# Performance work log

Measured on AMD Instinct MI355X. Metric: run time of the kernel, lower is better.

Reference implementation:

```python
import jax, jax.numpy as jnp
import numpy as np

N_HEADS = 12


def setup_inputs() -> dict:
    key = jax.random.key(0)
    ks = jax.random.split(key, 4)
    B, T, C = 1, 4096, 768
    x = jax.random.normal(ks[0], (B, T, C), dtype=jnp.float32)
    w_qkv = jax.random.normal(ks[1], (C, 3 * C), dtype=jnp.float32) * (C ** -0.5)
    b_qkv = jnp.zeros((3 * C,), dtype=jnp.float32)
    w_proj = jax.random.normal(ks[2], (C, C), dtype=jnp.float32) * (C ** -0.5)
    b_proj = jnp.zeros((C,), dtype=jnp.float32)
    return {"x": x, "w_qkv": w_qkv, "b_qkv": b_qkv, "w_proj": w_proj, "b_proj": b_proj}


def reference(x, w_qkv, b_qkv, w_proj, b_proj):
    B, T, C = x.shape
    H = N_HEADS
    hd = C // H
    qkv = x @ w_qkv + b_qkv                      # [B,T,3C]
    q, k, v = jnp.split(qkv, 3, axis=-1)
    # [B,H,T,hd]
    q = q.reshape(B, T, H, hd).transpose(0, 2, 1, 3)
    k = k.reshape(B, T, H, hd).transpose(0, 2, 1, 3)
    v = v.reshape(B, T, H, hd).transpose(0, 2, 1, 3)
    scale = 1.0 / jnp.sqrt(jnp.float32(hd))
    attn = jnp.einsum('bhqd,bhkd->bhqk', q, k) * scale  # [B,H,T,T]
    causal = jnp.tril(jnp.ones((T, T), dtype=bool))
    attn = jnp.where(causal, attn, jnp.float32(-jnp.inf))
    attn = jax.nn.softmax(attn, axis=-1)
    out = jnp.einsum('bhqk,bhkd->bhqd', attn, v)        # [B,H,T,hd]
    out = out.transpose(0, 2, 1, 3).reshape(B, T, C)
    return out @ w_proj + b_proj
```

## Files before the change

### kernel.cpp

```cpp
#include <hip/hip_runtime.h>
#include <hip/hip_bf16.h>


#define T_SEQ 4096
#define C_DIM 768
#define C3    2304
#define NH    12
#define HD    64

typedef __attribute__((ext_vector_type(8))) short bf16x8;
typedef __attribute__((ext_vector_type(4))) short bf16x4;
typedef __attribute__((ext_vector_type(4))) float f32x4;

__device__ inline unsigned short f2bf(float f) {
  union { float f; unsigned u; } v; v.f = f;
  unsigned r = v.u + 0x7fff + ((v.u >> 16) & 1);
  return (unsigned short)(r >> 16);
}
__device__ inline unsigned short f2bf_trunc(float f) {
  union { float f; unsigned u; } v; v.f = f;
  return (unsigned short)(v.u >> 16);
}

__device__ inline void gl2lds16(const void* g, void* l) {
  __builtin_amdgcn_global_load_lds(
      (const __attribute__((address_space(1))) unsigned int*)g,
      (__attribute__((address_space(3))) unsigned int*)l, 16, 0, 0);
}

#if __has_builtin(__builtin_amdgcn_exp2f)
#define EXP2F(x) __builtin_amdgcn_exp2f(x)
#else
#define EXP2F(x) exp2f(x)
#endif

#define NB_CONV  (T_SEQ * C_DIM / 2048)
#define NB_TQKV  ((C3 / 32) * (C_DIM / 32))
#define NB_TPROJ ((C_DIM / 32) * (C_DIM / 32))

__global__ __launch_bounds__(256) void prep_fused(
    const float* __restrict__ x, const float* __restrict__ w_qkv,
    const float* __restrict__ w_proj, unsigned short* __restrict__ xb,
    unsigned short* __restrict__ wqkvT, unsigned short* __restrict__ wprojT) {
  __shared__ float t[32][33];
  const int b = blockIdx.x;
  const int tid = threadIdx.x;

  if (b < NB_CONV) {
    int i = (b * 256 + tid) * 8;
    float4 v0 = *(const float4*)(x + i);
    float4 v1 = *(const float4*)(x + i + 4);
    unsigned short o[8] = {f2bf(v0.x), f2bf(v0.y), f2bf(v0.z), f2bf(v0.w),
                           f2bf(v1.x), f2bf(v1.y), f2bf(v1.z), f2bf(v1.w)};
    *(uint4*)(xb + i) = *(uint4*)o;
    return;
  }
  const float* in;
  unsigned short* outT;
  int R, Cc, bi;
  if (b < NB_CONV + NB_TQKV) {
    in = w_qkv; outT = wqkvT; R = C_DIM; Cc = C3; bi = b - NB_CONV;
  } else {
    in = w_proj; outT = wprojT; R = C_DIM; Cc = C_DIM; bi = b - NB_CONV - NB_TQKV;
  }
  const int tx = tid & 31, ty = tid >> 5;
  const int c0 = (bi % (Cc / 32)) * 32, r0 = (bi / (Cc / 32)) * 32;
#pragma unroll
  for (int i = 0; i < 4; ++i) {
    int r = ty + i * 8;
    t[r][tx] = in[(size_t)(r0 + r) * Cc + c0 + tx];
  }
  __syncthreads();
#pragma unroll
  for (int i = 0; i < 4; ++i) {
    int c = ty + i * 8;
    outT[(size_t)(c0 + c) * R + r0 + tx] = f2bf(t[tx][c]);
  }
}

__global__ __launch_bounds__(256) void gemm_qkv(
    const unsigned short* __restrict__ A, const unsigned short* __restrict__ Bt,
    const float* __restrict__ bias, unsigned short* __restrict__ Cq,
    unsigned short* __restrict__ vTp, int M, int N, int K) {
  __shared__ unsigned short As[128 * 64];
  __shared__ unsigned short Bs[128 * 64];
  const int tid = threadIdx.x;
  const int wave = tid >> 6, lane = tid & 63;
  const int lo = lane & 15, g8 = lane >> 4;
  const int lo7 = lo & 7;
  const int wm = wave >> 1, wn = wave & 1;
  const int bm = blockIdx.y * 128, bn = blockIdx.x * 128;
  const int drow8 = lane >> 3;
  const int dslot = (lane & 7) * 8;
  const int dsrc = ((lane & 7) ^ drow8) * 8;

  f32x4 acc[4][4];
#pragma unroll
  for (int mt = 0; mt < 4; ++mt)
#pragma unroll
    for (int nt = 0; nt < 4; ++nt) acc[mt][nt] = (f32x4){0.f, 0.f, 0.f, 0.f};

  const unsigned short* Abase = A + (size_t)bm * K;
  const unsigned short* Bbase = Bt + (size_t)bn * K;

  for (int k0 = 0; k0 < K; k0 += 64) {
    __syncthreads();
#pragma unroll
    for (int p = 0; p < 4; ++p) {
      const int r = p * 32 + wave * 8 + drow8;
      gl2lds16(Abase + (size_t)r * K + k0 + dsrc, As + r * 64 + dslot);
      gl2lds16(Bbase + (size_t)r * K + k0 + dsrc, Bs + r * 64 + dslot);
    }
    __syncthreads();

#pragma unroll
    for (int kk = 0; kk < 2; ++kk) {
      bf16x8 a[4], b[4];
#pragma unroll
      for (int mt = 0; mt < 4; ++mt)
        a[mt] = *(const bf16x8*)(
            As + (wm * 64 + mt * 16 + lo) * 64 + (((kk * 4 + g8) ^ lo7) * 8));
#pragma unroll
      for (int nt = 0; nt < 4; ++nt)
        b[nt] = *(const bf16x8*)(
            Bs + (wn * 64 + nt * 16 + lo) * 64 + (((kk * 4 + g8) ^ lo7) * 8));
#pragma unroll
      for (int mt = 0; mt < 4; ++mt)
#pragma unroll
        for (int nt = 0; nt < 4; ++nt)
          acc[mt][nt] = __builtin_amdgcn_mfma_f32_16x16x32_bf16(a[mt], b[nt], acc[mt][nt], 0, 0, 0);
    }
  }

  if (bn < 2 * C_DIM) {
#pragma unroll
    for (int nt = 0; nt < 4; ++nt) {
      const int n = bn + wn * 64 + nt * 16 + lo;
      const float bv = bias[n];
#pragma unroll
      for (int mt = 0; mt < 4; ++mt)
#pragma unroll
        for (int r = 0; r < 4; ++r) {
          const int m = bm + wm * 64 + mt * 16 + g8 * 4 + r;
          Cq[(size_t)m * C3 + n] = f2bf(acc[mt][nt][r] + bv);
        }
    }
  } else {
#pragma unroll
    for (int nt = 0; nt < 4; ++nt) {
      const int n = bn + wn * 64 + nt * 16 + lo;
      const float bv = bias[n];
      unsigned short* row = vTp + (size_t)(n - 2 * C_DIM) * T_SEQ;
#pragma unroll
      for (int mt = 0; mt < 4; ++mt) {
        const int mbase = (bm + wm * 64 + mt * 16 + g8 * 4) & ~31;
        bf16x4 o4;
#pragma unroll
        for (int r = 0; r < 4; ++r) o4[r] = (short)f2bf(acc[mt][nt][r] + bv);
        *(bf16x4*)(row + mbase + 8 * g8 + 4 * (mt & 1)) = o4;
      }
    }
  }
}

__global__ __launch_bounds__(256) void gemm_bt_mfma(
    const unsigned short* __restrict__ A, const unsigned short* __restrict__ Bt,
    const float* __restrict__ bias, float* __restrict__ C,
    int M, int N, int K) {
  __shared__ unsigned short As[128 * 64];
  __shared__ unsigned short Bs[128 * 64];
  const int tid = threadIdx.x;
  const int wave = tid >> 6, lane = tid & 63;
  const int lo = lane & 15, g8 = lane >> 4;
  const int lo7 = lo & 7;
  const int wm = wave >> 1, wn = wave & 1;
  const int bm = blockIdx.y * 128, bn = blockIdx.x * 128;
  const int drow8 = lane >> 3;
  const int dslot = (lane & 7) * 8;
  const int dsrc = ((lane & 7) ^ drow8) * 8;

  f32x4 acc[4][4];
#pragma unroll
  for (int mt = 0; mt < 4; ++mt)
#pragma unroll
    for (int nt = 0; nt < 4; ++nt) acc[mt][nt] = (f32x4){0.f, 0.f, 0.f, 0.f};

  const unsigned short* Abase = A + (size_t)bm * K;
  const unsigned short* Bbase = Bt + (size_t)bn * K;

  for (int k0 = 0; k0 < K; k0 += 64) {
    __syncthreads();
#pragma unroll
    for (int p = 0; p < 4; ++p) {
      const int r = p * 32 + wave * 8 + drow8;
      gl2lds16(Abase + (size_t)r * K + k0 + dsrc, As + r * 64 + dslot);
      gl2lds16(Bbase + (size_t)r * K + k0 + dsrc, Bs + r * 64 + dslot);
    }
    __syncthreads();

#pragma unroll
    for (int kk = 0; kk < 2; ++kk) {
      bf16x8 a[4], b[4];
#pragma unroll
      for (int mt = 0; mt < 4; ++mt)
        a[mt] = *(const bf16x8*)(
            As + (wm * 64 + mt * 16 + lo) * 64 + (((kk * 4 + g8) ^ lo7) * 8));
#pragma unroll
      for (int nt = 0; nt < 4; ++nt)
        b[nt] = *(const bf16x8*)(
            Bs + (wn * 64 + nt * 16 + lo) * 64 + (((kk * 4 + g8) ^ lo7) * 8));
#pragma unroll
      for (int mt = 0; mt < 4; ++mt)
#pragma unroll
        for (int nt = 0; nt < 4; ++nt)
          acc[mt][nt] = __builtin_amdgcn_mfma_f32_16x16x32_bf16(a[mt], b[nt], acc[mt][nt], 0, 0, 0);
    }
  }

#pragma unroll
  for (int nt = 0; nt < 4; ++nt) {
    const int n = bn + wn * 64 + nt * 16 + lo;
    const float bv = bias[n];
#pragma unroll
    for (int mt = 0; mt < 4; ++mt)
#pragma unroll
      for (int r = 0; r < 4; ++r) {
        const int m = bm + wm * 64 + mt * 16 + g8 * 4 + r;
        C[(size_t)m * N + n] = acc[mt][nt][r] + bv;
      }
  }
}

#define PO_SLOT ((size_t)NH * 64 * 4096)
#define PL_SLOT ((size_t)NH * 64 * 64)

__global__ __launch_bounds__(256) void flash_attn_split14(
    const unsigned short* __restrict__ qkv,
    const unsigned short* __restrict__ vTp,
    float* __restrict__ Po, float* __restrict__ Pl) {
  __shared__ unsigned short Ks[3][64 * 64];
  __shared__ unsigned short Vs[3][64 * 64];

  const int bid = blockIdx.x;
  const int xcd = bid & 7;
  const int j2 = bid >> 3;
  const int Hh = xcd * 3 + (j2 >> 5);
  const int h = Hh >> 1;
  const int s = Hh & 1;
  const int i = j2 & 31;
  const int j = 63 - i;
  const int nJ = s ? (31 - i) : 33;
  const int kJ0 = s ? 33 : 0;
  const int nI = s ? (i + 1) : 0;
  const int T = nJ + nI;

  const int tid = threadIdx.x;
  const int w = tid >> 6;
  const int lane = tid & 63;
  const int lo = lane & 15;
  const int g = lane >> 4;
  const int lo7 = lo & 7;
  const float qscale = 0.125f * 1.44269504f;

  const unsigned short* Kg = qkv + C_DIM + h * HD;
  const unsigned short* Vg = vTp + (size_t)(h * HD) * T_SEQ;

  const int drow = tid >> 3;
  const int dslot = (tid & 7) * 8;
  const int dsrc = ((tid & 7) ^ (drow & 7)) * 8;

  bf16x8 qbJ[2], qbI[2];
#pragma unroll
  for (int dh = 0; dh < 2; ++dh)
    qbJ[dh] = *(const bf16x8*)(
        qkv + (size_t)(j * 64 + w * 16 + lo) * C3 + h * HD + dh * 32 + g * 8);
#pragma unroll
  for (int dh = 0; dh < 2; ++dh)
    qbI[dh] = *(const bf16x8*)(
        qkv + (size_t)(i * 64 + w * 16 + lo) * C3 + h * HD + dh * 32 + g * 8);

  auto KT = [&](int t) { return t < nJ ? kJ0 + t : t - nJ; };

  {
    const int ka = KT(0), kb = KT(1);
#pragma unroll
    for (int p2 = 0; p2 < 2; ++p2) {
      const int r = p2 * 32 + drow;
      gl2lds16(Kg + (size_t)(ka * 64 + r) * C3 + dsrc, Ks[0] + r * 64 + dslot);
      gl2lds16(Vg + (size_t)r * T_SEQ + ka * 64 + dsrc, Vs[0] + r * 64 + dslot);
    }
#pragma unroll
    for (int p2 = 0; p2 < 2; ++p2) {
      const int r = p2 * 32 + drow;
      gl2lds16(Kg + (size_t)(kb * 64 + r) * C3 + dsrc, Ks[1] + r * 64 + dslot);
      gl2lds16(Vg + (size_t)r * T_SEQ + kb * 64 + dsrc, Vs[1] + r * 64 + dslot);
    }
    asm volatile("s_waitcnt vmcnt(4)" ::: "memory");
    __builtin_amdgcn_s_barrier();
  }

  float l_i = 0.f;
  f32x4 o_acc[4];
#pragma unroll
  for (int dt = 0; dt < 4; ++dt) o_acc[dt] = (f32x4){0.f, 0.f, 0.f, 0.f};

  int ic = 0;
  int iw = 2;
  int t = 0;

  auto body = [&](const bf16x8 (&qb)[2], int qtcur) __attribute__((always_inline)) {
    if (t + 2 < T) {
      const int k2 = KT(t + 2);
      unsigned short* Kd = Ks[iw];
      unsigned short* Vd = Vs[iw];
#pragma unroll
      for (int p2 = 0; p2 < 2; ++p2) {
        const int r = p2 * 32 + drow;
        gl2lds16(Kg + (size_t)(k2 * 64 + r) * C3 + dsrc, Kd + r * 64 + dslot);
        gl2lds16(Vg + (size_t)r * T_SEQ + k2 * 64 + dsrc, Vd + r * 64 + dslot);
      }
    }
    const unsigned short* Kc = Ks[ic];
    const unsigned short* Vc = Vs[ic];
    const int ktc = KT(t);

    f32x4 st[4];
#pragma unroll
    for (int mt = 0; mt < 4; ++mt) st[mt] = (f32x4){0.f, 0.f, 0.f, 0.f};
#pragma unroll
    for (int mt = 0; mt < 4; ++mt)
#pragma unroll
      for (int dh = 0; dh < 2; ++dh) {
        bf16x8 a = *(const bf16x8*)(
            Kc + (mt * 16 + lo) * 64 + (((dh * 4 + g) ^ lo7) * 8));
        st[mt] = __builtin_amdgcn_mfma_f32_16x16x32_bf16(a, qb[dh], st[mt], 0, 0, 0);
      }

    if (ktc == qtcur) {
      const int qloc = w * 16 + lo;
#pragma unroll
      for (int mt = 0; mt < 4; ++mt)
#pragma unroll
        for (int r = 0; r < 4; ++r)
          if (mt * 16 + g * 4 + r > qloc) st[mt][r] = -1e30f;
    }

    float lsum = 0.f;
    bf16x8 pt[2];
#pragma unroll
    for (int kh = 0; kh < 2; ++kh) {
#pragma unroll
      for (int jj = 0; jj < 4; ++jj) {
        float e0 = EXP2F(st[kh * 2][jj] * qscale);
        float e1 = EXP2F(st[kh * 2 + 1][jj] * qscale);
        lsum += e0 + e1;
        pt[kh][jj] = (short)f2bf_trunc(e0);
        pt[kh][4 + jj] = (short)f2bf_trunc(e1);
      }
    }
    l_i += lsum;

#pragma unroll
    for (int dt = 0; dt < 4; ++dt)
#pragma unroll
      for (int kh = 0; kh < 2; ++kh) {
        bf16x8 av = *(const bf16x8*)(
            Vc + (dt * 16 + lo) * 64 + (((kh * 4 + g) ^ lo7) * 8));
        o_acc[dt] = __builtin_amdgcn_mfma_f32_16x16x32_bf16(av, pt[kh], o_acc[dt], 0, 0, 0);
      }

    if (t + 2 < T)
      asm volatile("s_waitcnt vmcnt(4)" ::: "memory");
    else
      asm volatile("s_waitcnt vmcnt(0)" ::: "memory");
    __builtin_amdgcn_s_barrier();

    ic = (ic == 2) ? 0 : ic + 1;
    iw = (iw == 2) ? 0 : iw + 1;
    ++t;
  };

  auto flush = [&](int slot, int qt) __attribute__((always_inline)) {
    float lred = l_i + __shfl_xor(l_i, 16);
    lred += __shfl_xor(lred, 32);
    float* PoS = Po + ((size_t)slot * NH + h) * (64 * 4096) + (size_t)qt * 4096;
#pragma unroll
    for (int dt = 0; dt < 4; ++dt)
      *(f32x4*)(PoS + (w * 16 + lo) * 64 + dt * 16 + g * 4) = o_acc[dt];
    if (g == 0)
      Pl[(((size_t)slot * NH + h) * 64 + qt) * 64 + w * 16 + lo] = lred;
    l_i = 0.f;
#pragma unroll
    for (int dt = 0; dt < 4; ++dt) o_acc[dt] = (f32x4){0.f, 0.f, 0.f, 0.f};
  };

  for (int u = 0; u < nJ; ++u) body(qbJ, j);
  if (nJ > 0) flush(s, j);
  for (int u = 0; u < nI; ++u) body(qbI, i);
  if (nI > 0) flush(0, i);
}

__global__ __launch_bounds__(256) void combine_partials(
    const float* __restrict__ Po, const float* __restrict__ Pl,
    unsigned short* __restrict__ out) {
  const int bid = blockIdx.x;
  const int h = bid / 64, qt = bid % 64;
  const int tid = threadIdx.x;
  const int q = tid >> 2;
  const int c = (tid & 3) * 16;
  const bool two = (qt >= 33);
  const size_t sl = (size_t)h * 64 + qt;
  const float* P0 = Po + sl * 4096 + q * 64 + c;
  const float* P1 = P0 + PO_SLOT;
  float l = Pl[sl * 64 + q];
  if (two) l += Pl[PL_SLOT + sl * 64 + q];
  const float inv = 1.0f / l;
  unsigned short ob[16];
#pragma unroll
  for (int e = 0; e < 4; ++e) {
    f32x4 v = *(const f32x4*)(P0 + e * 4);
    if (two) {
      f32x4 v1 = *(const f32x4*)(P1 + e * 4);
      v += v1;
    }
#pragma unroll
    for (int r = 0; r < 4; ++r) ob[e * 4 + r] = f2bf(v[r] * inv);
  }
  unsigned short* o = out + (size_t)(qt * 64 + q) * C_DIM + h * 64 + c;
  *(uint4*)o = *(uint4*)ob;
  *(uint4*)(o + 8) = *(uint4*)(ob + 8);
}

extern "C" void kernel_launch(void* const* d_in, const int* in_sizes, int n_in,
                              void* d_out, int out_size, void* d_ws, size_t ws_size,
                              hipStream_t stream) {
  const float* x      = (const float*)d_in[0];
  const float* w_qkv  = (const float*)d_in[1];
  const float* b_qkv  = (const float*)d_in[2];
  const float* w_proj = (const float*)d_in[3];
  const float* b_proj = (const float*)d_in[4];
  float* out = (float*)d_out;

  unsigned short* xb     = (unsigned short*)d_ws;
  unsigned short* wqkvT  = xb + (size_t)T_SEQ * C_DIM;
  unsigned short* wprojT = wqkvT + (size_t)C3 * C_DIM;
  unsigned short* qkv    = wprojT + (size_t)C_DIM * C_DIM;
  unsigned short* vTp    = qkv + (size_t)T_SEQ * C3;
  unsigned short* attnb  = vTp + (size_t)C_DIM * T_SEQ;
  float* Po = (float*)(attnb + (size_t)T_SEQ * C_DIM);
  float* Pl = Po + 2 * PO_SLOT;

  prep_fused<<<NB_CONV + NB_TQKV + NB_TPROJ, 256, 0, stream>>>(
      x, w_qkv, w_proj, xb, wqkvT, wprojT);

  gemm_qkv<<<dim3(C3 / 128, T_SEQ / 128), 256, 0, stream>>>(
      xb, wqkvT, b_qkv, qkv, vTp, T_SEQ, C3, C_DIM);

  flash_attn_split14<<<T_SEQ / 64 * NH, 256, 0, stream>>>(qkv, vTp, Po, Pl);

  combine_partials<<<NH * 64, 256, 0, stream>>>(Po, Pl, attnb);

  gemm_bt_mfma<<<dim3(C_DIM / 128, T_SEQ / 128), 256, 0, stream>>>(
      attnb, wprojT, b_proj, out, T_SEQ, C_DIM, C_DIM);
}
```

Baseline: 180.6 us.

## Split attention work into three KV ranges per query pair with MFMA row sums

Attention work is re-split so each paired (i, 63-i) query-tile chain of 65 KV tiles is divided into three chunks of about 22 tiles. This gives 1152 blocks instead of 768, for better load balance and occupancy, and the combine step now merges up to three partials. The softmax scale and log2e are folded into Q in the QKV GEMM epilogue, and row sums are computed with an MFMA against a ones vector instead of scalar adds and shuffles. The LDS pipeline also drops from three to two buffers with full vmcnt(0) waits and adds s_setprio around the MFMA sections. The two-buffer pipeline exposes more load latency, and the extra partials increase combine traffic.

After: 186.4 us. 1.03x slower.

```diff
diff --git a/kernel.cpp b/kernel.cpp
--- a/kernel.cpp
+++ b/kernel.cpp
@@ -133,6 +133,7 @@
   }
 
   if (bn < 2 * C_DIM) {
+    const float sc = (bn < C_DIM) ? 0.18033688011112042f : 1.0f;
 #pragma unroll
     for (int nt = 0; nt < 4; ++nt) {
       const int n = bn + wn * 64 + nt * 16 + lo;
@@ -142,7 +143,7 @@
 #pragma unroll
         for (int r = 0; r < 4; ++r) {
           const int m = bm + wm * 64 + mt * 16 + g8 * 4 + r;
-          Cq[(size_t)m * C3 + n] = f2bf(acc[mt][nt][r] + bv);
+          Cq[(size_t)m * C3 + n] = f2bf((acc[mt][nt][r] + bv) * sc);
         }
     }
   } else {
@@ -233,25 +234,32 @@
 
 #define PO_SLOT ((size_t)NH * 64 * 4096)
 #define PL_SLOT ((size_t)NH * 64 * 64)
-
-__global__ __launch_bounds__(256) void flash_attn_split14(
+#define KSTEP   (64 * C3)
+
+__global__ __launch_bounds__(256) void flash_attn_split15(
     const unsigned short* __restrict__ qkv,
     const unsigned short* __restrict__ vTp,
     float* __restrict__ Po, float* __restrict__ Pl) {
-  __shared__ unsigned short Ks[3][64 * 64];
-  __shared__ unsigned short Vs[3][64 * 64];
+  __shared__ unsigned short Ks[2][64 * 64];
+  __shared__ unsigned short Vs[2][64 * 64];
 
   const int bid = blockIdx.x;
   const int xcd = bid & 7;
-  const int j2 = bid >> 3;
-  const int Hh = xcd * 3 + (j2 >> 5);
-  const int h = Hh >> 1;
-  const int s = Hh & 1;
-  const int i = j2 & 31;
-  const int j = 63 - i;
-  const int nJ = s ? (31 - i) : 33;
-  const int kJ0 = s ? 33 : 0;
-  const int nI = s ? (i + 1) : 0;
+  const int idx = xcd * 144 + (bid >> 3);
+  const int h = idx / 96;
+  const int rem = idx - h * 96;
+  const int s = rem >> 5;
+  const int i = rem & 31;
+  const int jt = 63 - i;
+  const int nJt = jt + 1;
+  const int u0 = (s == 0) ? 0 : (s == 1) ? 22 : 44;
+  const int u1 = (s == 0) ? 22 : (s == 1) ? 44 : 65;
+  const int jEnd = (u1 < nJt) ? u1 : nJt;
+  const int nJ = (jEnd > u0) ? (jEnd - u0) : 0;
+  const int kJ0 = u0;
+  const int iBeg = (u0 > nJt) ? u0 : nJt;
+  const int nI = (u1 > iBeg) ? (u1 - iBeg) : 0;
+  const int kI0 = iBeg - nJt;
   const int T = nJ + nI;
 
   const int tid = threadIdx.x;
@@ -260,7 +268,6 @@
   const int lo = lane & 15;
   const int g = lane >> 4;
   const int lo7 = lo & 7;
-  const float qscale = 0.125f * 1.44269504f;
 
   const unsigned short* Kg = qkv + C_DIM + h * HD;
   const unsigned short* Vg = vTp + (size_t)(h * HD) * T_SEQ;
@@ -268,65 +275,66 @@
   const int drow = tid >> 3;
   const int dslot = (tid & 7) * 8;
   const int dsrc = ((tid & 7) ^ (drow & 7)) * 8;
+  const size_t kOff = (size_t)drow * C3 + dsrc;
+  const size_t vOff = (size_t)drow * T_SEQ + dsrc;
 
   bf16x8 qbJ[2], qbI[2];
 #pragma unroll
   for (int dh = 0; dh < 2; ++dh)
     qbJ[dh] = *(const bf16x8*)(
-        qkv + (size_t)(j * 64 + w * 16 + lo) * C3 + h * HD + dh * 32 + g * 8);
+        qkv + (size_t)(jt * 64 + w * 16 + lo) * C3 + h * HD + dh * 32 + g * 8);
 #pragma unroll
   for (int dh = 0; dh < 2; ++dh)
     qbI[dh] = *(const bf16x8*)(
         qkv + (size_t)(i * 64 + w * 16 + lo) * C3 + h * HD + dh * 32 + g * 8);
 
-  auto KT = [&](int t) { return t < nJ ? kJ0 + t : t - nJ; };
-
-  {
-    const int ka = KT(0), kb = KT(1);
-#pragma unroll
-    for (int p2 = 0; p2 < 2; ++p2) {
-      const int r = p2 * 32 + drow;
-      gl2lds16(Kg + (size_t)(ka * 64 + r) * C3 + dsrc, Ks[0] + r * 64 + dslot);
-      gl2lds16(Vg + (size_t)r * T_SEQ + ka * 64 + dsrc, Vs[0] + r * 64 + dslot);
-    }
-#pragma unroll
-    for (int p2 = 0; p2 < 2; ++p2) {
-      const int r = p2 * 32 + drow;
-      gl2lds16(Kg + (size_t)(kb * 64 + r) * C3 + dsrc, Ks[1] + r * 64 + dslot);
-      gl2lds16(Vg + (size_t)r * T_SEQ + kb * 64 + dsrc, Vs[1] + r * 64 + dslot);
-    }
-    asm volatile("s_waitcnt vmcnt(4)" ::: "memory");
-    __builtin_amdgcn_s_barrier();
-  }
-
-  float l_i = 0.f;
+  const int k0t = (nJ > 0) ? kJ0 : kI0;
+  const unsigned short* pK0 = Kg + (size_t)k0t * KSTEP + kOff;
+  const unsigned short* pK1 = pK0 + (size_t)32 * C3;
+  const unsigned short* pV0 = Vg + (size_t)k0t * 64 + vOff;
+  const unsigned short* pV1 = pV0 + (size_t)32 * T_SEQ;
+  const unsigned short* iK0 = Kg + (size_t)kI0 * KSTEP + kOff;
+  const unsigned short* iK1 = iK0 + (size_t)32 * C3;
+  const unsigned short* iV0 = Vg + (size_t)kI0 * 64 + vOff;
+  const unsigned short* iV1 = iV0 + (size_t)32 * T_SEQ;
+
+  int nxt = 0;
+  auto stage = [&](int buf) __attribute__((always_inline)) {
+    gl2lds16(pK0, Ks[buf] + drow * 64 + dslot);
+    gl2lds16(pK1, Ks[buf] + (32 + drow) * 64 + dslot);
+    gl2lds16(pV0, Vs[buf] + drow * 64 + dslot);
+    gl2lds16(pV1, Vs[buf] + (32 + drow) * 64 + dslot);
+    ++nxt;
+    if (nxt == nJ) {
+      pK0 = iK0; pK1 = iK1; pV0 = iV0; pV1 = iV1;
+    } else {
+      pK0 += KSTEP; pK1 += KSTEP; pV0 += 64; pV1 += 64;
+    }
+  };
+
+  bf16x8 onesb;
+#pragma unroll
+  for (int e = 0; e < 8; ++e) onesb[e] = (short)0x3F80;
+
+  stage(0);
+  asm volatile("s_waitcnt vmcnt(0)" ::: "memory");
+  __builtin_amdgcn_s_barrier();
+
   f32x4 o_acc[4];
 #pragma unroll
   for (int dt = 0; dt < 4; ++dt) o_acc[dt] = (f32x4){0.f, 0.f, 0.f, 0.f};
-
-  int ic = 0;
-  int iw = 2;
-  int t = 0;
-
-  auto body = [&](const bf16x8 (&qb)[2], int qtcur) __attribute__((always_inline)) {
-    if (t + 2 < T) {
-      const int k2 = KT(t + 2);
-      unsigned short* Kd = Ks[iw];
-      unsigned short* Vd = Vs[iw];
-#pragma unroll
-      for (int p2 = 0; p2 < 2; ++p2) {
-        const int r = p2 * 32 + drow;
-        gl2lds16(Kg + (size_t)(k2 * 64 + r) * C3 + dsrc, Kd + r * 64 + dslot);
-        gl2lds16(Vg + (size_t)r * T_SEQ + k2 * 64 + dsrc, Vd + r * 64 + dslot);
-      }
-    }
-    const unsigned short* Kc = Ks[ic];
-    const unsigned short* Vc = Vs[ic];
-    const int ktc = KT(t);
+  f32x4 lacc = (f32x4){0.f, 0.f, 0.f, 0.f};
+  int cur = 0;
+
+  auto body = [&](const bf16x8 (&qb)[2], bool domask) __attribute__((always_inline)) {
+    if (nxt < T) stage(cur ^ 1);
+    const unsigned short* Kc = Ks[cur];
+    const unsigned short* Vc = Vs[cur];
 
     f32x4 st[4];
 #pragma unroll
     for (int mt = 0; mt < 4; ++mt) st[mt] = (f32x4){0.f, 0.f, 0.f, 0.f};
+    __builtin_amdgcn_s_setprio(1);
 #pragma unroll
     for (int mt = 0; mt < 4; ++mt)
 #pragma unroll
@@ -335,8 +343,9 @@
             Kc + (mt * 16 + lo) * 64 + (((dh * 4 + g) ^ lo7) * 8));
         st[mt] = __builtin_amdgcn_mfma_f32_16x16x32_bf16(a, qb[dh], st[mt], 0, 0, 0);
       }
-
-    if (ktc == qtcur) {
+    __builtin_amdgcn_s_setprio(0);
+
+    if (domask) {
       const int qloc = w * 16 + lo;
 #pragma unroll
       for (int mt = 0; mt < 4; ++mt)
@@ -345,21 +354,21 @@
           if (mt * 16 + g * 4 + r > qloc) st[mt][r] = -1e30f;
     }
 
-    float lsum = 0.f;
     bf16x8 pt[2];
 #pragma unroll
     for (int kh = 0; kh < 2; ++kh) {
 #pragma unroll
       for (int jj = 0; jj < 4; ++jj) {
-        float e0 = EXP2F(st[kh * 2][jj] * qscale);
-        float e1 = EXP2F(st[kh * 2 + 1][jj] * qscale);
-        lsum += e0 + e1;
+        float e0 = EXP2F(st[kh * 2][jj]);
+        float e1 = EXP2F(st[kh * 2 + 1][jj]);
         pt[kh][jj] = (short)f2bf_trunc(e0);
         pt[kh][4 + jj] = (short)f2bf_trunc(e1);
       }
     }
-    l_i += lsum;
-
+
+    __builtin_amdgcn_s_setprio(1);
+    lacc = __builtin_amdgcn_mfma_f32_16x16x32_bf16(onesb, pt[0], lacc, 0, 0, 0);
+    lacc = __builtin_amdgcn_mfma_f32_16x16x32_bf16(onesb, pt[1], lacc, 0, 0, 0);
 #pragma unroll
     for (int dt = 0; dt < 4; ++dt)
 #pragma unroll
@@ -368,36 +377,32 @@
             Vc + (dt * 16 + lo) * 64 + (((kh * 4 + g) ^ lo7) * 8));
         o_acc[dt] = __builtin_amdgcn_mfma_f32_16x16x32_bf16(av, pt[kh], o_acc[dt], 0, 0, 0);
       }
-
-    if (t + 2 < T)
-      asm volatile("s_waitcnt vmcnt(4)" ::: "memory");
-    else
-      asm volatile("s_waitcnt vmcnt(0)" ::: "memory");
+    __builtin_amdgcn_s_setprio(0);
+
+    asm volatile("s_waitcnt vmcnt(0)" ::: "memory");
     __builtin_amdgcn_s_barrier();
-
-    ic = (ic == 2) ? 0 : ic + 1;
-    iw = (iw == 2) ? 0 : iw + 1;
-    ++t;
+    cur ^= 1;
   };
 
   auto flush = [&](int slot, int qt) __attribute__((always_inline)) {
-    float lred = l_i + __shfl_xor(l_i, 16);
-    lred += __shfl_xor(lred, 32);
     float* PoS = Po + ((size_t)slot * NH + h) * (64 * 4096) + (size_t)qt * 4096;
 #pragma unroll
     for (int dt = 0; dt < 4; ++dt)
       *(f32x4*)(PoS + (w * 16 + lo) * 64 + dt * 16 + g * 4) = o_acc[dt];
     if (g == 0)
-      Pl[(((size_t)slot * NH + h) * 64 + qt) * 64 + w * 16 + lo] = lred;
-    l_i = 0.f;
+      Pl[(size_t)slot * PL_SLOT + ((size_t)h * 64 + qt) * 64 + w * 16 + lo] =
+          lacc[0];
 #pragma unroll
     for (int dt = 0; dt < 4; ++dt) o_acc[dt] = (f32x4){0.f, 0.f, 0.f, 0.f};
+    lacc = (f32x4){0.f, 0.f, 0.f, 0.f};
   };
 
-  for (int u = 0; u < nJ; ++u) body(qbJ, j);
-  if (nJ > 0) flush(s, j);
-  for (int u = 0; u < nI; ++u) body(qbI, i);
-  if (nI > 0) flush(0, i);
+  const bool jDiag = (kJ0 + nJ == nJt);
+  const bool iDiag = (nI > 0) && (kI0 + nI == i + 1);
+  for (int u = 0; u < nJ; ++u) body(qbJ, jDiag && (u == nJ - 1));
+  if (nJ > 0) flush(s, jt);
+  for (int u = 0; u < nI; ++u) body(qbI, iDiag && (u == nI - 1));
+  if (nI > 0) flush(s, i);
 }
 
 __global__ __launch_bounds__(256) void combine_partials(
@@ -408,21 +413,23 @@
   const int tid = threadIdx.x;
   const int q = tid >> 2;
   const int c = (tid & 3) * 16;
-  const bool two = (qt >= 33);
+  const bool v0 = (qt >= 32);
+  const bool v1 = (qt >= 21);
+  const bool v2 = (qt <= 31) || (qt >= 44);
   const size_t sl = (size_t)h * 64 + qt;
   const float* P0 = Po + sl * 4096 + q * 64 + c;
-  const float* P1 = P0 + PO_SLOT;
-  float l = Pl[sl * 64 + q];
-  if (two) l += Pl[PL_SLOT + sl * 64 + q];
+  float l = 0.f;
+  if (v0) l += Pl[sl * 64 + q];
+  if (v1) l += Pl[PL_SLOT + sl * 64 + q];
+  if (v2) l += Pl[2 * PL_SLOT + sl * 64 + q];
   const float inv = 1.0f / l;
   unsigned short ob[16];
 #pragma unroll
   for (int e = 0; e < 4; ++e) {
-    f32x4 v = *(const f32x4*)(P0 + e * 4);
-    if (two) {
-      f32x4 v1 = *(const f32x4*)(P1 + e * 4);
-      v += v1;
-    }
+    f32x4 v = (f32x4){0.f, 0.f, 0.f, 0.f};
+    if (v0) v += *(const f32x4*)(P0 + e * 4);
+    if (v1) v += *(const f32x4*)(P0 + PO_SLOT + e * 4);
+    if (v2) v += *(const f32x4*)(P0 + 2 * PO_SLOT + e * 4);
 #pragma unroll
     for (int r = 0; r < 4; ++r) ob[e * 4 + r] = f2bf(v[r] * inv);
   }
@@ -448,7 +455,7 @@
   unsigned short* vTp    = qkv + (size_t)T_SEQ * C3;
   unsigned short* attnb  = vTp + (size_t)C_DIM * T_SEQ;
   float* Po = (float*)(attnb + (size_t)T_SEQ * C_DIM);
-  float* Pl = Po + 2 * PO_SLOT;
+  float* Pl = Po + 3 * PO_SLOT;
 
   prep_fused<<<NB_CONV + NB_TQKV + NB_TPROJ, 256, 0, stream>>>(
       x, w_qkv, w_proj, xb, wqkvT, wprojT);
@@ -456,7 +463,7 @@
   gemm_qkv<<<dim3(C3 / 128, T_SEQ / 128), 256, 0, stream>>>(
       xb, wqkvT, b_qkv, qkv, vTp, T_SEQ, C3, C_DIM);
 
-  flash_attn_split14<<<T_SEQ / 64 * NH, 256, 0, stream>>>(qkv, vTp, Po, Pl);
+  flash_attn_split15<<<NH * 32 * 3, 256, 0, stream>>>(qkv, vTp, Po, Pl);
 
   combine_partials<<<NH * 64, 256, 0, stream>>>(Po, Pl, attnb);
 
```
